# Kernel tuning notes

Measured on AMD Instinct MI355X. Metric: run time of the kernel, lower is better.

## Reference

```python
import jax, jax.numpy as jnp
import numpy as np

EPS = 1e-9

def setup_inputs() -> dict:
    key = jax.random.key(0)
    k1, k2 = jax.random.split(key)
    B, D = 65536, 512
    e = jax.random.normal(k1, (B, D), dtype=jnp.float32)
    tau = jax.random.normal(k2, (B, D), dtype=jnp.float32)
    return {"e": e, "tau": tau}

def reference(e, tau):
    # Barlow Twins (diagonal-only) loss.
    # torch .std(dim=0) is unbiased (ddof=1).
    B = e.shape[0]
    e_norm = (e - e.mean(axis=0)) / (e.std(axis=0, ddof=1) + EPS)
    tau_norm = (tau - tau.mean(axis=0)) / (tau.std(axis=0, ddof=1) + EPS)
    # diag(e_norm.T @ tau_norm) / B == per-feature batch reduction of products
    c_diag = jnp.sum(e_norm * tau_norm, axis=0) / B
    return jnp.sum((1.0 - c_diag) ** 2)
```

## Files before the change

kernel.cpp:

```cpp
#include <hip/hip_runtime.h>

#define BT_D   512
#define BT_D4  128
#define NBLK   1024
#define NTHR   256
#define NWAVE  4
#define DEPTH  4

#define BT_ACC(ev, tv)                                                  \
    do {                                                                \
        se.x += (ev).x; se.y += (ev).y; se.z += (ev).z; se.w += (ev).w; \
        st.x += (tv).x; st.y += (tv).y; st.z += (tv).z; st.w += (tv).w; \
        se2.x = fmaf((ev).x, (ev).x, se2.x);                            \
        se2.y = fmaf((ev).y, (ev).y, se2.y);                            \
        se2.z = fmaf((ev).z, (ev).z, se2.z);                            \
        se2.w = fmaf((ev).w, (ev).w, se2.w);                            \
        st2.x = fmaf((tv).x, (tv).x, st2.x);                            \
        st2.y = fmaf((tv).y, (tv).y, st2.y);                            \
        st2.z = fmaf((tv).z, (tv).z, st2.z);                            \
        st2.w = fmaf((tv).w, (tv).w, st2.w);                            \
        set.x = fmaf((ev).x, (tv).x, set.x);                            \
        set.y = fmaf((ev).y, (tv).y, set.y);                            \
        set.z = fmaf((ev).z, (tv).z, set.z);                            \
        set.w = fmaf((ev).w, (tv).w, set.w);                            \
    } while (0)

#define BT_ADD4(dst, a) \
    do { (dst).x += (a).x; (dst).y += (a).y; (dst).z += (a).z; (dst).w += (a).w; } while (0)

#define BT_ISSUE(sidx, slot_)                                                     \
    do {                                                                          \
        unsigned _p = p0 + (sidx);                                                \
        if (_p >= pend) _p = pend - 1;    \
        const unsigned _c = (_p << 1) | par;                                      \
        const size_t _o = ((size_t)_c << 6) + (unsigned)lane;                     \
        __builtin_amdgcn_global_load_lds(                                         \
            (const __attribute__((address_space(1))) void*)(e4 + _o),            \
            (__attribute__((address_space(3))) void*)&buf_e[w][slot_][0],        \
            16, 0, 0);                                                            \
        __builtin_amdgcn_global_load_lds(                                         \
            (const __attribute__((address_space(1))) void*)(t4 + _o),            \
            (__attribute__((address_space(3))) void*)&buf_t[w][slot_][0],        \
            16, 0, 0);                                                            \
    } while (0)

__global__ __launch_bounds__(NTHR, 4) void bt_partial_kernel(
    const float4* __restrict__ e4, const float4* __restrict__ t4,
    float* __restrict__ acc, int B, int nslot)
{
    const int tid  = threadIdx.x;
    const int w    = tid >> 6;
    const int lane = tid & 63;

    __shared__ float4 buf_e[NWAVE][DEPTH][64];
    __shared__ float4 buf_t[NWAVE][DEPTH][64];

    float4 se  = make_float4(0.f, 0.f, 0.f, 0.f);
    float4 se2 = make_float4(0.f, 0.f, 0.f, 0.f);
    float4 st  = make_float4(0.f, 0.f, 0.f, 0.f);
    float4 st2 = make_float4(0.f, 0.f, 0.f, 0.f);
    float4 set = make_float4(0.f, 0.f, 0.f, 0.f);

    const unsigned npair  = (unsigned)B;
    const unsigned wg     = (unsigned)blockIdx.x * NWAVE + w;
    const unsigned par    = wg & 1u;
    const unsigned pairid = wg >> 1;
    const unsigned PW     = (NBLK * NWAVE) >> 1;
    const unsigned cpw    = (npair + PW - 1) / PW;
    const unsigned p0     = pairid * cpw;
    const unsigned pend   = (p0 + cpw < npair) ? (p0 + cpw) : npair;

    if (p0 < pend) {
        const unsigned steps = pend - p0;
        BT_ISSUE(0u, 0); BT_ISSUE(1u, 1); BT_ISSUE(2u, 2); BT_ISSUE(3u, 3);
        for (unsigned s = 0; s < steps; ++s) {
            const unsigned slot = s & (DEPTH - 1);
            asm volatile("s_waitcnt vmcnt(6)" ::: "memory");
            const float4 ev = buf_e[w][slot][lane];
            const float4 tv = buf_t[w][slot][lane];
            asm volatile("" ::: "memory");
            BT_ISSUE(s + DEPTH, slot);
            BT_ACC(ev, tv);
        }
    }
    asm volatile("s_waitcnt vmcnt(0)" ::: "memory");
    __syncthreads();

    float4 (*scr)[5] = (float4 (*)[5])&buf_e[0][0][0];
    if (w >= 2) {
        float4 (*L)[5] = scr + (w - 2) * 64;
        L[lane][0] = se;  L[lane][1] = se2; L[lane][2] = st;
        L[lane][3] = st2; L[lane][4] = set;
    }
    __syncthreads();
    if (w < 2) {
        float4 (*L)[5] = scr + w * 64;
        BT_ADD4(se,  L[lane][0]); BT_ADD4(se2, L[lane][1]);
        BT_ADD4(st,  L[lane][2]); BT_ADD4(st2, L[lane][3]);
        BT_ADD4(set, L[lane][4]);

        float* ap = acc + (size_t)(blockIdx.x & (nslot - 1)) * (5 * BT_D);
        const int col = (lane + (w << 6)) * 4;
        atomicAdd(&ap[0 * BT_D + col + 0], se.x);
        atomicAdd(&ap[0 * BT_D + col + 1], se.y);
        atomicAdd(&ap[0 * BT_D + col + 2], se.z);
        atomicAdd(&ap[0 * BT_D + col + 3], se.w);
        atomicAdd(&ap[1 * BT_D + col + 0], se2.x);
        atomicAdd(&ap[1 * BT_D + col + 1], se2.y);
        atomicAdd(&ap[1 * BT_D + col + 2], se2.z);
        atomicAdd(&ap[1 * BT_D + col + 3], se2.w);
        atomicAdd(&ap[2 * BT_D + col + 0], st.x);
        atomicAdd(&ap[2 * BT_D + col + 1], st.y);
        atomicAdd(&ap[2 * BT_D + col + 2], st.z);
        atomicAdd(&ap[2 * BT_D + col + 3], st.w);
        atomicAdd(&ap[3 * BT_D + col + 0], st2.x);
        atomicAdd(&ap[3 * BT_D + col + 1], st2.y);
        atomicAdd(&ap[3 * BT_D + col + 2], st2.z);
        atomicAdd(&ap[3 * BT_D + col + 3], st2.w);
        atomicAdd(&ap[4 * BT_D + col + 0], set.x);
        atomicAdd(&ap[4 * BT_D + col + 1], set.y);
        atomicAdd(&ap[4 * BT_D + col + 2], set.z);
        atomicAdd(&ap[4 * BT_D + col + 3], set.w);
    }
}

#define BT_FIN(Se_, Se2_, St_, St2_, Set_)                               \
    do {                                                                 \
        const double Se = (Se_), Se2 = (Se2_), St = (St_), St2 = (St2_), \
                     Set = (Set_);                                       \
        const double me = Se / Bd, mt = St / Bd;                         \
        double ve = (Se2 - Bd * me * me) / (Bd - 1.0);                   \
        double vt = (St2 - Bd * mt * mt) / (Bd - 1.0);                   \
        ve = ve > 0.0 ? ve : 0.0;                                        \
        vt = vt > 0.0 ? vt : 0.0;                                        \
        const double sd_e = sqrt(ve) + 1e-9;                             \
        const double sd_t = sqrt(vt) + 1e-9;                             \
        const double c = (Set - Bd * me * mt) / (sd_e * sd_t * Bd);      \
        vsum += (1.0 - c) * (1.0 - c);                                   \
    } while (0)

__global__ __launch_bounds__(512) void bt_final_kernel(
    const float* __restrict__ acc, float* __restrict__ out, int B, int nslot)
{
    const int t  = threadIdx.x;
    const int c4 = t & 127;
    const int q  = t >> 7;

    float4 S0 = make_float4(0.f, 0.f, 0.f, 0.f);
    float4 S1 = S0, S2 = S0, S3 = S0, S4 = S0;
    const float4* a4 = (const float4*)acc;
    for (int s = q; s < nslot; s += 4) {
        const float4* a = a4 + (size_t)s * (5 * BT_D4);
        float4 x;
        x = a[0 * BT_D4 + c4]; BT_ADD4(S0, x);
        x = a[1 * BT_D4 + c4]; BT_ADD4(S1, x);
        x = a[2 * BT_D4 + c4]; BT_ADD4(S2, x);
        x = a[3 * BT_D4 + c4]; BT_ADD4(S3, x);
        x = a[4 * BT_D4 + c4]; BT_ADD4(S4, x);
    }

    __shared__ float4 L[3][128][5];
    __shared__ double R[128];
    if (q) {
        L[q - 1][c4][0] = S0; L[q - 1][c4][1] = S1; L[q - 1][c4][2] = S2;
        L[q - 1][c4][3] = S3; L[q - 1][c4][4] = S4;
    }
    __syncthreads();
    if (q == 0) {
        for (int j = 0; j < 3; ++j) {
            BT_ADD4(S0, L[j][c4][0]); BT_ADD4(S1, L[j][c4][1]);
            BT_ADD4(S2, L[j][c4][2]); BT_ADD4(S3, L[j][c4][3]);
            BT_ADD4(S4, L[j][c4][4]);
        }
        const double Bd = (double)B;
        double vsum = 0.0;
        BT_FIN(S0.x, S1.x, S2.x, S3.x, S4.x);
        BT_FIN(S0.y, S1.y, S2.y, S3.y, S4.y);
        BT_FIN(S0.z, S1.z, S2.z, S3.z, S4.z);
        BT_FIN(S0.w, S1.w, S2.w, S3.w, S4.w);
        R[c4] = vsum;
    }
    __syncthreads();
    for (int s2 = 64; s2 > 0; s2 >>= 1) {
        if (t < s2) R[t] += R[t + s2];
        __syncthreads();
    }
    if (t == 0) out[0] = (float)R[0];
}

extern "C" void kernel_launch(void* const* d_in, const int* in_sizes, int n_in,
                              void* d_out, int out_size, void* d_ws, size_t ws_size,
                              hipStream_t stream) {
    const float* e   = (const float*)d_in[0];
    const float* tau = (const float*)d_in[1];
    const int B = in_sizes[0] / BT_D;
    float* acc = (float*)d_ws;

    int nslot = 1;
    const size_t slot_bytes = (size_t)5 * BT_D * sizeof(float);
    if (ws_size >= 32 * slot_bytes)      nslot = 32;
    else if (ws_size >= 8 * slot_bytes)  nslot = 8;
    else if (ws_size >= 4 * slot_bytes)  nslot = 4;
    else if (ws_size >= 2 * slot_bytes)  nslot = 2;

    (void)hipMemsetAsync(d_ws, 0, (size_t)nslot * slot_bytes, stream);

    bt_partial_kernel<<<NBLK, NTHR, 0, stream>>>(
        (const float4*)e, (const float4*)tau, acc, B, nslot);
    bt_final_kernel<<<1, 512, 0, stream>>>(acc, (float*)d_out, B, nslot);
}
```

Baseline: 308.9 us.

## Fuse final reduction into partial kernel and use direct nontemporal grid-stride loads

Replaces the LDS-staged global_load_lds pipeline with plain grid-stride nontemporal float4 loads, unrolled by two, at 512 threads per block. The finalization kernel is merged into the main kernel through a last-block-done atomic counter, which removes one kernel launch. The in-block reduction is restructured for 4 row groups. This risks losing the explicit prefetch depth of the old LDS pipeline, and it adds a threadfence plus a counter atomic in every block.

```diff
diff --git a/kernel.cpp b/kernel.cpp
--- a/kernel.cpp
+++ b/kernel.cpp
@@ -3,9 +3,9 @@
 #define BT_D   512
 #define BT_D4  128
 #define NBLK   1024
-#define NTHR   256
-#define NWAVE  4
-#define DEPTH  4
+#define NTHR   512
+
+typedef float nf4 __attribute__((ext_vector_type(4)));
 
 #define BT_ACC(ev, tv)                                                  \
     do {                                                                \
@@ -28,32 +28,29 @@
 #define BT_ADD4(dst, a) \
     do { (dst).x += (a).x; (dst).y += (a).y; (dst).z += (a).z; (dst).w += (a).w; } while (0)
 
-#define BT_ISSUE(sidx, slot_)                                                     \
-    do {                                                                          \
-        unsigned _p = p0 + (sidx);                                                \
-        if (_p >= pend) _p = pend - 1;    \
-        const unsigned _c = (_p << 1) | par;                                      \
-        const size_t _o = ((size_t)_c << 6) + (unsigned)lane;                     \
-        __builtin_amdgcn_global_load_lds(                                         \
-            (const __attribute__((address_space(1))) void*)(e4 + _o),            \
-            (__attribute__((address_space(3))) void*)&buf_e[w][slot_][0],        \
-            16, 0, 0);                                                            \
-        __builtin_amdgcn_global_load_lds(                                         \
-            (const __attribute__((address_space(1))) void*)(t4 + _o),            \
-            (__attribute__((address_space(3))) void*)&buf_t[w][slot_][0],        \
-            16, 0, 0);                                                            \
+#define BT_FIN(Se_, Se2_, St_, St2_, Set_)                               \
+    do {                                                                 \
+        const double Se = (Se_), Se2 = (Se2_), St = (St_), St2 = (St2_), \
+                     Set = (Set_);                                       \
+        const double me = Se / Bd, mt = St / Bd;                         \
+        double ve = (Se2 - Bd * me * me) / (Bd - 1.0);                   \
+        double vt = (St2 - Bd * mt * mt) / (Bd - 1.0);                   \
+        ve = ve > 0.0 ? ve : 0.0;                                        \
+        vt = vt > 0.0 ? vt : 0.0;                                        \
+        const double sd_e = sqrt(ve) + 1e-9;                             \
+        const double sd_t = sqrt(vt) + 1e-9;                             \
+        const double c = (Set - Bd * me * mt) / (sd_e * sd_t * Bd);      \
+        vsum += (1.0 - c) * (1.0 - c);                                   \
     } while (0)
 
-__global__ __launch_bounds__(NTHR, 4) void bt_partial_kernel(
-    const float4* __restrict__ e4, const float4* __restrict__ t4,
-    float* __restrict__ acc, int B, int nslot)
+__global__ __launch_bounds__(NTHR, 8) void bt_fused_kernel(
+    const nf4* __restrict__ e4, const nf4* __restrict__ t4,
+    float* __restrict__ acc, unsigned* __restrict__ cnt,
+    float* __restrict__ out, int B, int nslot)
 {
-    const int tid  = threadIdx.x;
-    const int w    = tid >> 6;
-    const int lane = tid & 63;
-
-    __shared__ float4 buf_e[NWAVE][DEPTH][64];
-    __shared__ float4 buf_t[NWAVE][DEPTH][64];
+    const int tid = threadIdx.x;
+    const int c4  = tid & (BT_D4 - 1);
+    const int r   = tid >> 7;
 
     float4 se  = make_float4(0.f, 0.f, 0.f, 0.f);
     float4 se2 = make_float4(0.f, 0.f, 0.f, 0.f);
@@ -61,46 +58,52 @@
     float4 st2 = make_float4(0.f, 0.f, 0.f, 0.f);
     float4 set = make_float4(0.f, 0.f, 0.f, 0.f);
 
-    const unsigned npair  = (unsigned)B;
-    const unsigned wg     = (unsigned)blockIdx.x * NWAVE + w;
-    const unsigned par    = wg & 1u;
-    const unsigned pairid = wg >> 1;
-    const unsigned PW     = (NBLK * NWAVE) >> 1;
-    const unsigned cpw    = (npair + PW - 1) / PW;
-    const unsigned p0     = pairid * cpw;
-    const unsigned pend   = (p0 + cpw < npair) ? (p0 + cpw) : npair;
-
-    if (p0 < pend) {
-        const unsigned steps = pend - p0;
-        BT_ISSUE(0u, 0); BT_ISSUE(1u, 1); BT_ISSUE(2u, 2); BT_ISSUE(3u, 3);
-        for (unsigned s = 0; s < steps; ++s) {
-            const unsigned slot = s & (DEPTH - 1);
-            asm volatile("s_waitcnt vmcnt(6)" ::: "memory");
-            const float4 ev = buf_e[w][slot][lane];
-            const float4 tv = buf_t[w][slot][lane];
-            asm volatile("" ::: "memory");
-            BT_ISSUE(s + DEPTH, slot);
-            BT_ACC(ev, tv);
-        }
-    }
-    asm volatile("s_waitcnt vmcnt(0)" ::: "memory");
-    __syncthreads();
-
-    float4 (*scr)[5] = (float4 (*)[5])&buf_e[0][0][0];
-    if (w >= 2) {
-        float4 (*L)[5] = scr + (w - 2) * 64;
-        L[lane][0] = se;  L[lane][1] = se2; L[lane][2] = st;
-        L[lane][3] = st2; L[lane][4] = set;
-    }
-    __syncthreads();
-    if (w < 2) {
-        float4 (*L)[5] = scr + w * 64;
-        BT_ADD4(se,  L[lane][0]); BT_ADD4(se2, L[lane][1]);
-        BT_ADD4(st,  L[lane][2]); BT_ADD4(st2, L[lane][3]);
-        BT_ADD4(set, L[lane][4]);
+    const unsigned T  = (unsigned)gridDim.x * NTHR;
+    const unsigned N4 = (unsigned)B * BT_D4;
+    unsigned i = (unsigned)blockIdx.x * NTHR + tid;
+
+    for (; i + T < N4; i += 2u * T) {
+        const nf4 e0 = __builtin_nontemporal_load(e4 + i);
+        const nf4 t0 = __builtin_nontemporal_load(t4 + i);
+        const nf4 e1 = __builtin_nontemporal_load(e4 + i + T);
+        const nf4 t1 = __builtin_nontemporal_load(t4 + i + T);
+        BT_ACC(e0, t0);
+        BT_ACC(e1, t1);
+    }
+    for (; i < N4; i += T) {
+        const nf4 ev = __builtin_nontemporal_load(e4 + i);
+        const nf4 tv = __builtin_nontemporal_load(t4 + i);
+        BT_ACC(ev, tv);
+    }
+
+    __shared__ float4  L[3][BT_D4][5];
+    __shared__ double  R[BT_D4];
+    __shared__ unsigned lastblk;
+
+    if (r >= 2) {
+        float4 (*Lp)[5] = L[r - 2];
+        Lp[c4][0] = se;  Lp[c4][1] = se2; Lp[c4][2] = st;
+        Lp[c4][3] = st2; Lp[c4][4] = set;
+    }
+    __syncthreads();
+    if (r < 2) {
+        float4 (*Lp)[5] = L[r];
+        BT_ADD4(se,  Lp[c4][0]); BT_ADD4(se2, Lp[c4][1]); BT_ADD4(st, Lp[c4][2]);
+        BT_ADD4(st2, Lp[c4][3]); BT_ADD4(set, Lp[c4][4]);
+    }
+    __syncthreads();
+    if (r == 1) {
+        L[0][c4][0] = se;  L[0][c4][1] = se2; L[0][c4][2] = st;
+        L[0][c4][3] = st2; L[0][c4][4] = set;
+    }
+    __syncthreads();
+    if (r == 0) {
+        BT_ADD4(se,  L[0][c4][0]); BT_ADD4(se2, L[0][c4][1]);
+        BT_ADD4(st,  L[0][c4][2]); BT_ADD4(st2, L[0][c4][3]);
+        BT_ADD4(set, L[0][c4][4]);
 
         float* ap = acc + (size_t)(blockIdx.x & (nslot - 1)) * (5 * BT_D);
-        const int col = (lane + (w << 6)) * 4;
+        const int col = c4 * 4;
         atomicAdd(&ap[0 * BT_D + col + 0], se.x);
         atomicAdd(&ap[0 * BT_D + col + 1], se.y);
         atomicAdd(&ap[0 * BT_D + col + 2], se.z);
@@ -122,30 +125,17 @@
         atomicAdd(&ap[4 * BT_D + col + 2], set.z);
         atomicAdd(&ap[4 * BT_D + col + 3], set.w);
     }
-}
-
-#define BT_FIN(Se_, Se2_, St_, St2_, Set_)                               \
-    do {                                                                 \
-        const double Se = (Se_), Se2 = (Se2_), St = (St_), St2 = (St2_), \
-                     Set = (Set_);                                       \
-        const double me = Se / Bd, mt = St / Bd;                         \
-        double ve = (Se2 - Bd * me * me) / (Bd - 1.0);                   \
-        double vt = (St2 - Bd * mt * mt) / (Bd - 1.0);                   \
-        ve = ve > 0.0 ? ve : 0.0;                                        \
-        vt = vt > 0.0 ? vt : 0.0;                                        \
-        const double sd_e = sqrt(ve) + 1e-9;                             \
-        const double sd_t = sqrt(vt) + 1e-9;                             \
-        const double c = (Set - Bd * me * mt) / (sd_e * sd_t * Bd);      \
-        vsum += (1.0 - c) * (1.0 - c);                                   \
-    } while (0)
-
-__global__ __launch_bounds__(512) void bt_final_kernel(
-    const float* __restrict__ acc, float* __restrict__ out, int B, int nslot)
-{
-    const int t  = threadIdx.x;
-    const int c4 = t & 127;
-    const int q  = t >> 7;
-
+
+    __threadfence();
+    __syncthreads();
+    if (tid == 0)
+        lastblk = (atomicAdd(cnt, 1u) == (unsigned)(NBLK - 1)) ? 1u : 0u;
+    __syncthreads();
+    if (!lastblk) return;
+    __threadfence();
+    asm volatile("" ::: "memory");
+
+    const int q = tid >> 7;
     float4 S0 = make_float4(0.f, 0.f, 0.f, 0.f);
     float4 S1 = S0, S2 = S0, S3 = S0, S4 = S0;
     const float4* a4 = (const float4*)acc;
@@ -158,9 +148,6 @@
         x = a[3 * BT_D4 + c4]; BT_ADD4(S3, x);
         x = a[4 * BT_D4 + c4]; BT_ADD4(S4, x);
     }
-
-    __shared__ float4 L[3][128][5];
-    __shared__ double R[128];
     if (q) {
         L[q - 1][c4][0] = S0; L[q - 1][c4][1] = S1; L[q - 1][c4][2] = S2;
         L[q - 1][c4][3] = S3; L[q - 1][c4][4] = S4;
@@ -182,10 +169,10 @@
     }
     __syncthreads();
     for (int s2 = 64; s2 > 0; s2 >>= 1) {
-        if (t < s2) R[t] += R[t + s2];
+        if (tid < s2) R[tid] += R[tid + s2];
         __syncthreads();
     }
-    if (t == 0) out[0] = (float)R[0];
+    if (tid == 0) out[0] = (float)R[0];
 }
 
 extern "C" void kernel_launch(void* const* d_in, const int* in_sizes, int n_in,
@@ -198,14 +185,16 @@
 
     int nslot = 1;
     const size_t slot_bytes = (size_t)5 * BT_D * sizeof(float);
-    if (ws_size >= 32 * slot_bytes)      nslot = 32;
-    else if (ws_size >= 8 * slot_bytes)  nslot = 8;
-    else if (ws_size >= 4 * slot_bytes)  nslot = 4;
-    else if (ws_size >= 2 * slot_bytes)  nslot = 2;
-
-    (void)hipMemsetAsync(d_ws, 0, (size_t)nslot * slot_bytes, stream);
-
-    bt_partial_kernel<<<NBLK, NTHR, 0, stream>>>(
-        (const float4*)e, (const float4*)tau, acc, B, nslot);
-    bt_final_kernel<<<1, 512, 0, stream>>>(acc, (float*)d_out, B, nslot);
+    if (ws_size >= 32 * slot_bytes + 16)      nslot = 32;
+    else if (ws_size >= 8 * slot_bytes + 16)  nslot = 8;
+    else if (ws_size >= 4 * slot_bytes + 16)  nslot = 4;
+    else if (ws_size >= 2 * slot_bytes + 16)  nslot = 2;
+
+    unsigned* cnt = (unsigned*)((char*)d_ws + (size_t)nslot * slot_bytes);
+
+    (void)hipMemsetAsync(d_ws, 0, (size_t)nslot * slot_bytes + 16, stream);
+
+    bt_fused_kernel<<<NBLK, NTHR, 0, stream>>>(
+        (const nf4*)e, (const nf4*)tau, acc, cnt,
+        (float*)d_out, B, nslot);
 }
```

After: 565.9 us. 83.2% more time.
